# Performance work log

Hardware: AMD Instinct MI355X
Metric: run time of the kernel (lower is better)

The kernel has to match this reference:

```python
import jax, jax.numpy as jnp
import numpy as np

DIM = 1024
HEADS = 16
DIM_HEAD = 64
DIM_INNER = HEADS * DIM_HEAD  # 1024
SEQ = 2048
BATCH = 1


def setup_inputs() -> dict:
    key = jax.random.key(0)
    k1, k2, k3 = jax.random.split(key, 3)
    x = jax.random.normal(k1, (BATCH, SEQ, DIM), dtype=jnp.float32)
    # LinearNoBias(dim, 6*dim_inner): stored as [dim, 6*dim_inner] so fwd is x @ W
    W_qkv = jax.random.normal(k2, (DIM, 6 * DIM_INNER), dtype=jnp.float32) * (DIM ** -0.5)
    W_out = jax.random.normal(k3, (DIM_INNER, DIM), dtype=jnp.float32) * (DIM_INNER ** -0.5)
    return {"x": x, "W_qkv": W_qkv, "W_out": W_out}


def reference(x, W_qkv, W_out):
    b, n, _ = x.shape
    scale = DIM_HEAD ** -0.5

    qkv = x @ W_qkv  # [b, n, 6*h*d]
    qkv = qkv.reshape(b, n, 6, HEADS, DIM_HEAD).transpose(2, 0, 3, 1, 4)  # [6, b, h, n, d]
    qu, ku, vu, qc, kc, vc = qkv

    qc_s = qc * scale
    qu_s = qu * scale

    # strictly-upper-triangular causal mask (True above diagonal)
    causal_mask = jnp.triu(jnp.ones((n, n), dtype=bool), 1)

    # term1: lower-triangular (incl. diag) of qc_s @ vu^T
    term1 = jnp.einsum('bhid,bhjd->bhij', qc_s, vu)
    term1 = jnp.where(causal_mask, 0.0, term1)

    # lookahead: sigmoid of qu_s @ ku^T, strictly upper kept
    lookahead = jax.nn.sigmoid(jnp.einsum('bhid,bhjd->bhij', qu_s, ku))
    lookahead = jnp.where(causal_mask, lookahead, 0.0)

    # Su = term1 @ lookahead^T  (n x n by n x n matmul per head)
    Su = jnp.einsum('bhij,bhkj->bhik', term1, lookahead)

    Sc = jnp.einsum('bhid,bhjd->bhij', qc_s, kc)
    scores = Sc - jax.nn.silu(Su)
    scores = jnp.where(causal_mask, -jnp.inf, scores)

    attn = jax.nn.softmax(scores, axis=-1)
    out = jnp.einsum('bhij,bhjd->bhid', attn, vc)  # [b, h, n, d]

    out = out.transpose(0, 2, 1, 3).reshape(b, n, DIM_INNER)
    return out @ W_out
```

## Files before the change

kernel.cpp:

```cpp
#include <hip/hip_runtime.h>
#include <math.h>

typedef _Float16 f16;
typedef _Float16 f16x4 __attribute__((ext_vector_type(4)));
typedef _Float16 f16x8 __attribute__((ext_vector_type(8)));
typedef float f32x4 __attribute__((ext_vector_type(4)));

#define SEQ   2048
#define DIM   1024
#define NH    16
#define DH    64
#define NCOLS 6144
#define NHSD  (NH*SEQ*DH)
#define NTILE 136
#define MAXS  9
#define SLOTS_PER_HEAD 64

__device__ __forceinline__ int ns2(int a) {
  const int NS2[8] = {1,1,2,3,4,5,7,9};
  return NS2[a];
}
__device__ __forceinline__ int slot_base(int I) {
  const int PF[16] = {0,1,2,3,4,6,8,11,14,18,22,27,32,39,46,55};
  return PF[I];
}

__global__ __launch_bounds__(256) void k_tcast(const float* __restrict__ in, f16* __restrict__ out,
                                               int R, int C) {
  __shared__ f16 t[64 * 66];
  int bc = blockIdx.x, br = blockIdx.y;
  for (int it = 0; it < 16; ++it) {
    int idx = it * 256 + threadIdx.x;
    int r = idx >> 6, c = idx & 63;
    t[r * 66 + c] = (f16)in[(size_t)(br * 64 + r) * C + bc * 64 + c];
  }
  __syncthreads();
  for (int it = 0; it < 16; ++it) {
    int idx = it * 256 + threadIdx.x;
    int oc = idx >> 6, orr = idx & 63;
    out[(size_t)(bc * 64 + oc) * R + br * 64 + orr] = t[orr * 66 + oc];
  }
}

__global__ __launch_bounds__(256) void k_prepA(const float* __restrict__ x, f16* __restrict__ xhT) {
  int kt = blockIdx.x, by = blockIdx.y;
  f16* dst = xhT + ((size_t)(by * 16 + kt) << 13);
  int tid = threadIdx.x;
#pragma unroll
  for (int i = 0; i < 4; ++i) {
    int idx = i * 256 + tid;
    int chunk = idx >> 6, lane = idx & 63;
    int rb = chunk & 7, ks = chunk >> 3;
    int row = by * 128 + rb * 16 + (lane & 15);
    int kk = kt * 64 + ks * 32 + ((lane >> 4) << 3);
    const float* p = x + (size_t)row * DIM + kk;
    float4 lo = *(const float4*)p, hi = *(const float4*)(p + 4);
    f16x8 h;
    h[0] = (f16)lo.x; h[1] = (f16)lo.y; h[2] = (f16)lo.z; h[3] = (f16)lo.w;
    h[4] = (f16)hi.x; h[5] = (f16)hi.y; h[6] = (f16)hi.z; h[7] = (f16)hi.w;
    *(f16x8*)(dst + (size_t)idx * 8) = h;
  }
}

__global__ __launch_bounds__(256) void k_prepB(const float* __restrict__ Wq, f16* __restrict__ WqTf) {
  int kt = blockIdx.x, bx = blockIdx.y;
  f16* dst = WqTf + ((size_t)(bx * 16 + kt) << 13);
  int tid = threadIdx.x;
#pragma unroll
  for (int i = 0; i < 4; ++i) {
    int idx = i * 256 + tid;
    int chunk = idx >> 6, lane = idx & 63;
    int rb = chunk & 7, ks = chunk >> 3;
    int n = bx * 128 + rb * 16 + (lane & 15);
    int kk = kt * 64 + ks * 32 + ((lane >> 4) << 3);
    f16x8 h;
#pragma unroll
    for (int j = 0; j < 8; ++j) h[j] = (f16)Wq[(size_t)(kk + j) * NCOLS + n];
    *(f16x8*)(dst + (size_t)idx * 8) = h;
  }
}

__global__ __launch_bounds__(256) void k_gemm_qkv(const f16* __restrict__ xhT, const f16* __restrict__ WqTf,
                                                  f16* __restrict__ q6, f16* __restrict__ vuF) {
  __shared__ f16 sa[8192];
  __shared__ f16 sb[8192];
  int bx = blockIdx.x, by = blockIdx.y;
  int tid = threadIdx.x, w = tid >> 6, l = tid & 63, q = l >> 4, c = l & 15;
  f32x4 acc[2][8];
  const f32x4 zf = {0.f, 0.f, 0.f, 0.f};
  for (int i = 0; i < 2; ++i) for (int j = 0; j < 8; ++j) acc[i][j] = zf;

  for (int kt = 0; kt < 16; ++kt) {
    const f16* ta = xhT + ((size_t)(by * 16 + kt) << 13);
    const f16* tb = WqTf + ((size_t)(bx * 16 + kt) << 13);
    __syncthreads();
#pragma unroll
    for (int i = 0; i < 4; ++i) {
      int e = (i * 256 + tid) * 8;
      __builtin_amdgcn_global_load_lds((const __attribute__((address_space(1))) void*)(ta + e),
                                       (__attribute__((address_space(3))) void*)(sa + e), 16, 0, 0);
      __builtin_amdgcn_global_load_lds((const __attribute__((address_space(1))) void*)(tb + e),
                                       (__attribute__((address_space(3))) void*)(sb + e), 16, 0, 0);
    }
    __syncthreads();
#pragma unroll
    for (int ks = 0; ks < 2; ++ks) {
      f16x8 af[2], bf[8];
#pragma unroll
      for (int tr = 0; tr < 2; ++tr)
        af[tr] = *(const f16x8*)(sa + ((ks * 8 + w * 2 + tr) * 64 + l) * 8);
#pragma unroll
      for (int tc = 0; tc < 8; ++tc)
        bf[tc] = *(const f16x8*)(sb + ((ks * 8 + tc) * 64 + l) * 8);
#pragma unroll
      for (int tr = 0; tr < 2; ++tr)
#pragma unroll
        for (int tc = 0; tc < 8; ++tc)
          acc[tr][tc] = __builtin_amdgcn_mfma_f32_16x16x32_f16(af[tr], bf[tc], acc[tr][tc], 0, 0, 0);
    }
  }
#pragma unroll
  for (int tr = 0; tr < 2; ++tr)
#pragma unroll
    for (int tc = 0; tc < 8; ++tc)
#pragma unroll
      for (int r = 0; r < 4; ++r) {
        int row = by * 128 + w * 32 + tr * 16 + q * 4 + r;
        int col = bx * 128 + tc * 16 + c;
        float v = acc[tr][tc][r];
        int t = col >> 10, head = (col >> 6) & 15, dh = col & 63;
        if (t == 0 || t == 3) v *= 0.125f;
        f16 hv = (f16)v;
        if (t == 4) {
          size_t addr = (size_t)4 * NHSD + (size_t)head * (SEQ * DH) + ((size_t)(row >> 7) << 13)
                      + (size_t)(((((dh >> 5) << 3) + ((row >> 4) & 7)) * 64
                                  + ((((dh >> 3) & 3) << 4) | (row & 15))) * 8 + (dh & 7));
          q6[addr] = hv;
        } else if (t == 5) {
          size_t addr = (size_t)5 * NHSD + (size_t)head * (SEQ * DH) + ((size_t)(row >> 7) << 13)
                      + (size_t)((((((row >> 5) & 3) << 2) + (dh >> 4)) * 64
                                  + ((((row >> 3) & 3) << 4) | (dh & 15))) * 8 + (row & 7));
          q6[addr] = hv;
        } else if (t == 2) {
          q6[(size_t)2 * NHSD + (size_t)(head * SEQ + row) * DH + dh] = hv;
          size_t fa = ((size_t)(row >> 7) << 13)
                    + (size_t)((((((row >> 5) & 3) << 2) + (dh >> 4)) * 64
                                + ((((row >> 3) & 3) << 4) | (dh & 15))) * 8 + (row & 7));
          vuF[(size_t)head * (SEQ * DH) + fa] = hv;
        } else {
          q6[(size_t)t * NHSD + (size_t)(head * SEQ + row) * DH + dh] = hv;
        }
      }
}

__global__ __launch_bounds__(256) void k_t1lk(const f16* __restrict__ q6, f16* __restrict__ t1dT,
                                              f16* __restrict__ lkT) {
  __shared__ f16 st[128 * 128];
  int head = blockIdx.x / 152;
  int p = blockIdx.x % 152;
  bool is_lk = (p >= 16);
  int RB, CB;
  f16* dst;
  if (is_lk) {
    int p2 = p - 16;
    int K = 0, off = 0;
    while (off + (16 - K) <= p2) { off += 16 - K; ++K; }
    RB = K; CB = K + (p2 - off);
    dst = lkT + ((size_t)(head * NTILE + p2) << 14);
  } else {
    RB = p; CB = p;
    dst = t1dT + ((size_t)(head * 16 + p) << 14);
  }
  const f16* Ah = q6 + (size_t)(is_lk ? 0 : 3) * NHSD + (size_t)head * SEQ * DH;
  const f16* Bh = q6 + (size_t)(is_lk ? 1 : 2) * NHSD + (size_t)head * SEQ * DH;
  int tid = threadIdx.x, w = tid >> 6, l = tid & 63, q = l >> 4, c = l & 15;
  const f32x4 zf = {0.f, 0.f, 0.f, 0.f};
  f32x4 tacc[2][8];
  for (int tr = 0; tr < 2; ++tr) for (int tc = 0; tc < 8; ++tc) tacc[tr][tc] = zf;
#pragma unroll
  for (int ks = 0; ks < 2; ++ks) {
    f16x8 aq[2], bf[8];
#pragma unroll
    for (int tr = 0; tr < 2; ++tr)
      aq[tr] = *(const f16x8*)(Ah + (size_t)(RB * 128 + w * 32 + tr * 16 + c) * DH + ks * 32 + q * 8);
#pragma unroll
    for (int tc = 0; tc < 8; ++tc)
      bf[tc] = *(const f16x8*)(Bh + (size_t)(CB * 128 + tc * 16 + c) * DH + ks * 32 + q * 8);
#pragma unroll
    for (int tr = 0; tr < 2; ++tr)
#pragma unroll
      for (int tc = 0; tc < 8; ++tc)
        tacc[tr][tc] = __builtin_amdgcn_mfma_f32_16x16x32_f16(aq[tr], bf[tc], tacc[tr][tc], 0, 0, 0);
  }
#pragma unroll
  for (int tr = 0; tr < 2; ++tr)
#pragma unroll
    for (int tc = 0; tc < 8; ++tc)
#pragma unroll
      for (int r = 0; r < 4; ++r) {
        int row = w * 32 + tr * 16 + q * 4 + r;
        int col = tc * 16 + c;
        int rg = RB * 128 + row, cg = CB * 128 + col;
        float v = tacc[tr][tc][r];
        f16 ov;
        if (is_lk) ov = (cg > rg) ? (f16)__builtin_amdgcn_rcpf(1.f + __expf(-v)) : (f16)(0.f);
        else       ov = (cg <= rg) ? (f16)v : (f16)(0.f);
        st[(row << 7) + (((col >> 3) ^ (row & 15)) << 3) + (col & 7)] = ov;
      }
  __syncthreads();
#pragma unroll
  for (int i = 0; i < 8; ++i) {
    int ch = i * 256 + tid;
    int ks = ch >> 9, rb = (ch >> 6) & 7, ln = ch & 63;
    int qq = ln >> 4, cc = ln & 15;
    int row = rb * 16 + cc, cchunk = ks * 4 + qq;
    f16x8 v = *(const f16x8*)(st + (row << 7) + ((cchunk ^ (row & 15)) << 3));
    *(f16x8*)(dst + (size_t)ch * 8) = v;
  }
}

__global__ __launch_bounds__(256) void k_prefix(const f16* __restrict__ lkT, const f16* __restrict__ vuF,
                                                f16* __restrict__ PPT) {
  __shared__ f16 lkb[2][16384];
  __shared__ f16 vub[2][8192];
  __shared__ f16 st[8192];
  int head = blockIdx.x >> 4, K = blockIdx.x & 15;
  int offK = 16 * K - (K * (K - 1)) / 2;
  const f16* lkh = lkT + ((size_t)(head * NTILE) << 14);
  const f16* vuh = vuF + (size_t)head * (SEQ * DH);
  f16* pph = PPT + ((size_t)(head * NTILE) << 13);
  int tid = threadIdx.x, w = tid >> 6, l = tid & 63, q = l >> 4, c = l & 15;
  f32x4 acc[2][4];
  const f32x4 zf = {0.f, 0.f, 0.f, 0.f};
  for (int tr = 0; tr < 2; ++tr) for (int tv = 0; tv < 4; ++tv) acc[tr][tv] = zf;
  {
    const f16* lt = lkh + ((size_t)offK << 14);
#pragma unroll
    for (int i = 0; i < 8; ++i) {
      int e = (i * 256 + tid) * 8;
      __builtin_amdgcn_global_load_lds((const __attribute__((address_space(1))) void*)(lt + e),
                                       (__attribute__((address_space(3))) void*)(&lkb[0][0] + e), 16, 0, 0);
    }
    const f16* vt_ = vuh + ((size_t)K << 13);
#pragma unroll
    for (int i = 0; i < 4; ++i) {
      int e = (i * 256 + tid) * 8;
      __builtin_amdgcn_global_load_lds((const __attribute__((address_space(1))) void*)(vt_ + e),
                                       (__attribute__((address_space(3))) void*)(&vub[0][0] + e), 16, 0, 0);
    }
  }
  int pb = 0;
  for (int J = K; J < 16; ++J) {
    __syncthreads();
    if (J < 15) {
      const f16* lt = lkh + ((size_t)(offK + (J + 1 - K)) << 14);
#pragma unroll
      for (int i = 0; i < 8; ++i) {
        int e = (i * 256 + tid) * 8;
        __builtin_amdgcn_global_load_lds((const __attribute__((address_space(1))) void*)(lt + e),
                                         (__attribute__((address_space(3))) void*)(&lkb[pb ^ 1][0] + e), 16, 0, 0);
      }
      const f16* vt_ = vuh + ((size_t)(J + 1) << 13);
#pragma unroll
      for (int i = 0; i < 4; ++i) {
        int e = (i * 256 + tid) * 8;
        __builtin_amdgcn_global_load_lds((const __attribute__((address_space(1))) void*)(vt_ + e),
                                         (__attribute__((address_space(3))) void*)(&vub[pb ^ 1][0] + e), 16, 0, 0);
      }
    }
#pragma unroll
    for (int ks = 0; ks < 4; ++ks) {
      f16x8 af[2], bf[4];
#pragma unroll
      for (int tr = 0; tr < 2; ++tr)
        af[tr] = *(const f16x8*)(&lkb[pb][0] + ((ks * 8 + w * 2 + tr) * 64 + l) * 8);
#pragma unroll
      for (int tv = 0; tv < 4; ++tv)
        bf[tv] = *(const f16x8*)(&vub[pb][0] + ((ks * 4 + tv) * 64 + l) * 8);
#pragma unroll
      for (int tr = 0; tr < 2; ++tr)
#pragma unroll
        for (int tv = 0; tv < 4; ++tv)
          acc[tr][tv] = __builtin_amdgcn_mfma_f32_16x16x32_f16(af[tr], bf[tv], acc[tr][tv], 0, 0, 0);
    }
#pragma unroll
    for (int tr = 0; tr < 2; ++tr)
#pragma unroll
      for (int tv = 0; tv < 4; ++tv)
#pragma unroll
        for (int r = 0; r < 4; ++r) {
          int row = w * 32 + tr * 16 + q * 4 + r;
          int col = tv * 16 + c;
          st[(row << 6) + (((col >> 3) ^ (row & 7)) << 3) + (col & 7)] = (f16)acc[tr][tv][r];
        }
    __syncthreads();
    f16* dst = pph + ((size_t)(offK + (J - K)) << 13);
#pragma unroll
    for (int i = 0; i < 4; ++i) {
      int slot = i * 256 + tid;
      int chunk = slot >> 6, ln = slot & 63;
      int ks2 = chunk >> 3, tc = chunk & 7, qq = ln >> 4, cc = ln & 15;
      int row = tc * 16 + cc, cch = ks2 * 4 + qq;
      f16x8 v = *(const f16x8*)(st + (row << 6) + ((cch ^ (row & 7)) << 3));
      *(f16x8*)(dst + (size_t)slot * 8) = v;
    }
    pb ^= 1;
  }
}

__global__ __launch_bounds__(512, 1) void k_flash(const f16* __restrict__ q6, const f16* __restrict__ t1dT,
                                                  const f16* __restrict__ lkT, const f16* __restrict__ PPT,
                                                  f16* __restrict__ pO, float* __restrict__ pML) {
  __shared__ f16 Sb[2][40960];
  int bid = blockIdx.x;
  int big = bid & 1;
  int rest = bid >> 1;
  int head = ((rest & 7) << 1) | ((rest >> 3) & 1);
  int r2 = 31 - (rest >> 4);
  int a = 0, s = 0;
  {
    int acc = 0;
    for (int aa = 0; aa < 8; ++aa) {
      int si = ns2(aa);
      if (r2 >= acc && r2 < acc + si) { a = aa; s = r2 - acc; }
      acc += si;
    }
  }
  int I1 = 2 * a + 1;
  int S_ = ns2(a);
  int Ktot = I1 + 1;
  int K0 = (Ktot * s) / S_, K1 = (Ktot * (s + 1)) / S_;
  int IB = 2 * a + big;
  int Kbeg = (K0 < IB + 1) ? K0 : IB + 1;
  int Kend = (K1 < IB + 1) ? K1 : IB + 1;

  const f16* qc  = q6 + (size_t)3 * NHSD + (size_t)head * SEQ * DH;
  const f16* kcF = q6 + (size_t)4 * NHSD + (size_t)head * (SEQ * DH);
  const f16* vtF = q6 + (size_t)5 * NHSD + (size_t)head * (SEQ * DH);
  int tid = threadIdx.x, w = tid >> 6, l = tid & 63, q = l >> 4, c = l & 15;
  const f16* lkh = lkT + ((size_t)(head * NTILE) << 14);
  const f16* pph = PPT + ((size_t)(head * NTILE) << 13);
  const f16* t1d = t1dT + ((size_t)(head * 16 + IB) << 14);

  f16x8 a_qc[2];
#pragma unroll
  for (int ks = 0; ks < 2; ++ks)
    a_qc[ks] = *(const f16x8*)(qc + (size_t)(IB * 128 + w * 16 + c) * DH + ks * 32 + q * 8);
  f16x8 a_t1[4];
#pragma unroll
  for (int ks = 0; ks < 4; ++ks)
    a_t1[ks] = *(const f16x8*)(t1d + (size_t)((ks * 8 + w) * 64 + l) * 8);

  f32x4 su[8], oacc[4];
  float m_i[4], l_i[4];
  const f32x4 zf = {0.f, 0.f, 0.f, 0.f};
  for (int tv = 0; tv < 4; ++tv) oacc[tv] = zf;
  for (int r = 0; r < 4; ++r) { m_i[r] = -INFINITY; l_i[r] = 0.f; }

  if (Kbeg < Kend) {
    int K = Kbeg;
    int offK = 16 * K - (K * (K - 1)) / 2;
    f16* D = &Sb[0][0];
    const f16* p1 = lkh + ((size_t)(offK + (IB - K)) << 14);
#pragma unroll
    for (int i = 0; i < 4; ++i) {
      int e = (i * 512 + tid) * 8;
      __builtin_amdgcn_global_load_lds((const __attribute__((address_space(1))) void*)(p1 + e),
                                       (__attribute__((address_space(3))) void*)(D + e), 16, 0, 0);
    }
    if (K < IB) {
      const f16* pp = pph + ((size_t)(offK + (IB - 1 - K)) << 13);
#pragma unroll
      for (int i = 0; i < 2; ++i) {
        int e = (i * 512 + tid) * 8;
        __builtin_amdgcn_global_load_lds((const __attribute__((address_space(1))) void*)(pp + e),
                                         (__attribute__((address_space(3))) void*)(D + 16384 + e), 16, 0, 0);
      }
    }
    const f16* kt_ = kcF + ((size_t)K << 13);
    const f16* vv_ = vtF + ((size_t)K << 13);
#pragma unroll
    for (int i = 0; i < 2; ++i) {
      int e = (i * 512 + tid) * 8;
      __builtin_amdgcn_global_load_lds((const __attribute__((address_space(1))) void*)(kt_ + e),
                                       (__attribute__((address_space(3))) void*)(D + 24576 + e), 16, 0, 0);
      __builtin_amdgcn_global_load_lds((const __attribute__((address_space(1))) void*)(vv_ + e),
                                       (__attribute__((address_space(3))) void*)(D + 32768 + e), 16, 0, 0);
    }
  }

  int cur = 0;
  for (int K = Kbeg; K < Kend; ++K) {
#pragma unroll
    for (int tc = 0; tc < 8; ++tc) su[tc] = zf;

    __syncthreads();

    if (K + 1 < Kend) {
      int Kn = K + 1;
      int offKn = 16 * Kn - (Kn * (Kn - 1)) / 2;
      f16* D = &Sb[cur ^ 1][0];
      const f16* p1 = lkh + ((size_t)(offKn + (IB - Kn)) << 14);
#pragma unroll
      for (int i = 0; i < 4; ++i) {
        int e = (i * 512 + tid) * 8;
        __builtin_amdgcn_global_load_lds((const __attribute__((address_space(1))) void*)(p1 + e),
                                         (__attribute__((address_space(3))) void*)(D + e), 16, 0, 0);
      }
      if (Kn < IB) {
        const f16* pp = pph + ((size_t)(offKn + (IB - 1 - Kn)) << 13);
#pragma unroll
        for (int i = 0; i < 2; ++i) {
          int e = (i * 512 + tid) * 8;
          __builtin_amdgcn_global_load_lds((const __attribute__((address_space(1))) void*)(pp + e),
                                           (__attribute__((address_space(3))) void*)(D + 16384 + e), 16, 0, 0);
        }
      }
      const f16* kt_ = kcF + ((size_t)Kn << 13);
      const f16* vv_ = vtF + ((size_t)Kn << 13);
#pragma unroll
      for (int i = 0; i < 2; ++i) {
        int e = (i * 512 + tid) * 8;
        __builtin_amdgcn_global_load_lds((const __attribute__((address_space(1))) void*)(kt_ + e),
                                         (__attribute__((address_space(3))) void*)(D + 24576 + e), 16, 0, 0);
        __builtin_amdgcn_global_load_lds((const __attribute__((address_space(1))) void*)(vv_ + e),
                                         (__attribute__((address_space(3))) void*)(D + 32768 + e), 16, 0, 0);
      }
    }

    f16* bufc = &Sb[cur][0];
    if (K < IB) {
      const f16* ppb = bufc + 16384;
#pragma unroll
      for (int ks = 0; ks < 2; ++ks) {
        f16x8 bf[8];
#pragma unroll
        for (int tc = 0; tc < 8; ++tc)
          bf[tc] = *(const f16x8*)(ppb + ((ks * 8 + tc) * 64 + l) * 8);
#pragma unroll
        for (int tc = 0; tc < 8; ++tc)
          su[tc] = __builtin_amdgcn_mfma_f32_16x16x32_f16(a_qc[ks], bf[tc], su[tc], 0, 0, 0);
      }
    }
    {
      __builtin_amdgcn_s_setprio(1);
#pragma unroll
      for (int ks = 0; ks < 4; ++ks) {
        f16x8 bf[8];
#pragma unroll
        for (int tc = 0; tc < 8; ++tc)
          bf[tc] = *(const f16x8*)(bufc + ((ks * 8 + tc) * 64 + l) * 8);
#pragma unroll
        for (int tc = 0; tc < 8; ++tc)
          su[tc] = __builtin_amdgcn_mfma_f32_16x16x32_f16(a_t1[ks], bf[tc], su[tc], 0, 0, 0);
      }
      __builtin_amdgcn_s_setprio(0);
    }
#pragma unroll
    for (int tc = 0; tc < 8; ++tc)
#pragma unroll
      for (int r = 0; r < 4; ++r) {
        float v = su[tc][r];
        su[tc][r] = -v * __builtin_amdgcn_rcpf(1.f + __expf(-v));
      }
    {
      const f16* skc = bufc + 24576;
#pragma unroll
      for (int ks = 0; ks < 2; ++ks) {
        f16x8 bk[8];
#pragma unroll
        for (int tc = 0; tc < 8; ++tc)
          bk[tc] = *(const f16x8*)(skc + ((ks * 8 + tc) * 64 + l) * 8);
#pragma unroll
        for (int tc = 0; tc < 8; ++tc)
          su[tc] = __builtin_amdgcn_mfma_f32_16x16x32_f16(a_qc[ks], bk[tc], su[tc], 0, 0, 0);
      }
    }
    if (K == IB) {
#pragma unroll
      for (int tc = 0; tc < 8; ++tc)
#pragma unroll
        for (int r = 0; r < 4; ++r) {
          int rg = w * 16 + q * 4 + r;
          int cg = tc * 16 + c;
          if (cg > rg) su[tc][r] = -INFINITY;
        }
    }
#pragma unroll
    for (int r = 0; r < 4; ++r) {
      float mx = su[0][r];
#pragma unroll
      for (int tc = 1; tc < 8; ++tc) mx = fmaxf(mx, su[tc][r]);
      mx = fmaxf(mx, __shfl_xor(mx, 1)); mx = fmaxf(mx, __shfl_xor(mx, 2));
      mx = fmaxf(mx, __shfl_xor(mx, 4)); mx = fmaxf(mx, __shfl_xor(mx, 8));
      float mnew  = fmaxf(m_i[r], mx);
      float alpha = __expf(m_i[r] - mnew);
      float ssum = 0.f;
#pragma unroll
      for (int tc = 0; tc < 8; ++tc) {
        float pp = __expf(su[tc][r] - mnew);
        su[tc][r] = pp;
        ssum += pp;
      }
      ssum += __shfl_xor(ssum, 1); ssum += __shfl_xor(ssum, 2);
      ssum += __shfl_xor(ssum, 4); ssum += __shfl_xor(ssum, 8);
      l_i[r] = l_i[r] * alpha + ssum;
      m_i[r] = mnew;
#pragma unroll
      for (int tv = 0; tv < 4; ++tv) oacc[tv][r] *= alpha;
    }
    asm volatile("s_waitcnt lgkmcnt(0)" ::: "memory");
    __builtin_amdgcn_sched_barrier(0);
    __builtin_amdgcn_s_barrier();
    __builtin_amdgcn_sched_barrier(0);
#pragma unroll
    for (int tc = 0; tc < 8; ++tc)
#pragma unroll
      for (int r = 0; r < 4; ++r) {
        int row = w * 16 + q * 4 + r;
        int col = tc * 16 + c;
        bufc[(row << 7) + (((col >> 3) ^ (row & 15)) << 3) + (col & 7)] = (f16)su[tc][r];
      }
    {
      const f16* svt = bufc + 32768;
#pragma unroll
      for (int ks = 0; ks < 4; ++ks) {
        int ck = ks * 4 + q;
        f16x8 ap, bv[4];
        ap = *(const f16x8*)(bufc + ((w * 16 + c) << 7) + ((ck ^ c) << 3));
#pragma unroll
        for (int tv = 0; tv < 4; ++tv)
          bv[tv] = *(const f16x8*)(svt + ((ks * 4 + tv) * 64 + l) * 8);
#pragma unroll
        for (int tv = 0; tv < 4; ++tv)
          oacc[tv] = __builtin_amdgcn_mfma_f32_16x16x32_f16(ap, bv[tv], oacc[tv], 0, 0, 0);
      }
    }
    cur ^= 1;
  }

  int slot = head * SLOTS_PER_HEAD + slot_base(IB) + s;
  f16* po = pO + (size_t)slot * (128 * 64);
  float* pml = pML + (size_t)slot * 256;
  if (c == 0) {
#pragma unroll
    for (int r = 0; r < 4; ++r) {
      int row = w * 16 + q * 4 + r;
      pml[row] = m_i[r];
      pml[128 + row] = l_i[r];
    }
  }
#pragma unroll
  for (int tv = 0; tv < 4; ++tv)
#pragma unroll
    for (int r = 0; r < 4; ++r) {
      int row = w * 16 + q * 4 + r;
      int col = tv * 16 + c;
      po[row * 64 + col] = (f16)oacc[tv][r];
    }
}

__global__ __launch_bounds__(256) void k_merge(const f16* __restrict__ pO, const float* __restrict__ pML,
                                               f16* __restrict__ oh) {
  int head = blockIdx.x >> 4, I = blockIdx.x & 15;
  int S_ = ns2(I >> 1);
  int tid = threadIdx.x;
  int row = tid >> 1, half = tid & 1;
  int base = head * SLOTS_PER_HEAD + slot_base(I);
  float m[MAXS], lv[MAXS];
  float mstar = -INFINITY;
#pragma unroll
  for (int s = 0; s < MAXS; ++s)
    if (s < S_) {
      m[s] = pML[(size_t)(base + s) * 256 + row];
      lv[s] = pML[(size_t)(base + s) * 256 + 128 + row];
      mstar = fmaxf(mstar, m[s]);
    }
  float wt[MAXS];
  float lsum = 0.f;
#pragma unroll
  for (int s = 0; s < MAXS; ++s)
    if (s < S_) {
      wt[s] = __expf(m[s] - mstar);
      lsum += lv[s] * wt[s];
    }
  float rinv = __builtin_amdgcn_rcpf(lsum);
#pragma unroll
  for (int cc = 0; cc < 32; cc += 8) {
    float acc[8] = {0.f, 0.f, 0.f, 0.f, 0.f, 0.f, 0.f, 0.f};
#pragma unroll
    for (int s = 0; s < MAXS; ++s)
      if (s < S_) {
        f16x8 v = *(const f16x8*)(pO + (size_t)(base + s) * 8192 + row * 64 + half * 32 + cc);
#pragma unroll
        for (int e = 0; e < 8; ++e) acc[e] += wt[s] * (float)v[e];
      }
    f16x8 o;
#pragma unroll
    for (int e = 0; e < 8; ++e) o[e] = (f16)(acc[e] * rinv);
    *(f16x8*)(oh + (size_t)(I * 128 + row) * DIM + head * 64 + half * 32 + cc) = o;
  }
}

__global__ __launch_bounds__(256) void k_gemm_out(const f16* __restrict__ A, const f16* __restrict__ B,
                                                  float* __restrict__ out) {
  __shared__ f16 sa[128 * 72];
  __shared__ f16 sb[128 * 72];
  int bx = blockIdx.x, by = blockIdx.y;
  int tid = threadIdx.x, w = tid >> 6, l = tid & 63, q = l >> 4, c = l & 15;
  f32x4 acc[2][8];
  const f32x4 zf = {0.f, 0.f, 0.f, 0.f};
  for (int i = 0; i < 2; ++i) for (int j = 0; j < 8; ++j) acc[i][j] = zf;
  for (int kt = 0; kt < DIM / 64; ++kt) {
    __syncthreads();
#pragma unroll
    for (int it = 0; it < 4; ++it) {
      int idx = it * 256 + tid; int r = idx >> 3, ch = idx & 7;
      *(float4*)(sa + r * 72 + ch * 8) = *(const float4*)(A + (size_t)(by * 128 + r) * DIM + kt * 64 + ch * 8);
      *(float4*)(sb + r * 72 + ch * 8) = *(const float4*)(B + (size_t)(bx * 128 + r) * DIM + kt * 64 + ch * 8);
    }
    __syncthreads();
#pragma unroll
    for (int ks = 0; ks < 2; ++ks) {
      f16x8 af[2], bf[8];
#pragma unroll
      for (int tr = 0; tr < 2; ++tr) af[tr] = *(const f16x8*)(sa + (w * 32 + tr * 16 + c) * 72 + ks * 32 + q * 8);
#pragma unroll
      for (int tc = 0; tc < 8; ++tc) bf[tc] = *(const f16x8*)(sb + (tc * 16 + c) * 72 + ks * 32 + q * 8);
#pragma unroll
      for (int tr = 0; tr < 2; ++tr)
#pragma unroll
        for (int tc = 0; tc < 8; ++tc)
          acc[tr][tc] = __builtin_amdgcn_mfma_f32_16x16x32_f16(af[tr], bf[tc], acc[tr][tc], 0, 0, 0);
    }
  }
#pragma unroll
  for (int tr = 0; tr < 2; ++tr)
#pragma unroll
    for (int tc = 0; tc < 8; ++tc)
#pragma unroll
      for (int r = 0; r < 4; ++r) {
        int row = by * 128 + w * 32 + tr * 16 + q * 4 + r;
        int col = bx * 128 + tc * 16 + c;
        out[(size_t)row * DIM + col] = acc[tr][tc][r];
      }
}

extern "C" void kernel_launch(void* const* d_in, const int* in_sizes, int n_in,
                              void* d_out, int out_size, void* d_ws, size_t ws_size,
                              hipStream_t stream) {
  const float* x  = (const float*)d_in[0];
  const float* Wq = (const float*)d_in[1];
  const float* Wo = (const float*)d_in[2];
  float* out = (float*)d_out;

  f16* ws = (f16*)d_ws;
  size_t off = 0;
  f16* q6   = ws + off; off += (size_t)6 * NHSD;
  f16* vuF  = ws + off; off += (size_t)NHSD;
  f16* xhT  = ws + off; off += (size_t)SEQ * DIM;
  f16* WqTf = ws + off; off += (size_t)NCOLS * DIM;
  f16* WoT  = ws + off; off += (size_t)DIM * DIM;
  f16* oh   = ws + off; off += (size_t)SEQ * DIM;
  f16* pO   = ws + off; off += (size_t)NH * SLOTS_PER_HEAD * 128 * 64;
  f16* lkT  = ws + off; off += (size_t)NH * NTILE * 128 * 128;
  f16* t1dT = ws + off; off += (size_t)NH * 16 * 128 * 128;
  f16* PPT  = ws + off; off += (size_t)NH * NTILE * 128 * 64;
  float* pML = (float*)(ws + off); off += (size_t)NH * SLOTS_PER_HEAD * 256 * 2;

  k_prepA<<<dim3(16, 16), 256, 0, stream>>>(x, xhT);
  k_prepB<<<dim3(16, 48), 256, 0, stream>>>(Wq, WqTf);
  k_tcast<<<dim3(DIM / 64, DIM / 64), 256, 0, stream>>>(Wo, WoT, DIM, DIM);
  k_gemm_qkv<<<dim3(NCOLS / 128, SEQ / 128), 256, 0, stream>>>(xhT, WqTf, q6, vuF);
  k_t1lk<<<NH * 152, 256, 0, stream>>>(q6, t1dT, lkT);
  k_prefix<<<NH * 16, 256, 0, stream>>>(lkT, vuF, PPT);
  k_flash<<<NH * 64, 512, 0, stream>>>(q6, t1dT, lkT, PPT, pO, pML);
  k_merge<<<NH * 16, 256, 0, stream>>>(pO, pML, oh);
  k_gemm_out<<<dim3(DIM / 128, SEQ / 128), 256, 0, stream>>>(oh, WoT, out);
}
```

Baseline: 315.2 us.

## Fuse weight/input prep kernels and coalesce Wq transpose; narrow output GEMM tiles

Merges the three preprocessing kernels (x cast, W_qkv transpose-cast, W_out transpose-cast) into one launch dispatched by block index, which removes two kernel launches. The W_qkv transpose now reads rows with coalesced float4 loads and transposes through shared memory, replacing the previous strided per-element global reads. The output GEMM tile shrinks from 128x128 to 128x64, doubling the grid from 128 to 256 blocks so more CUs are busy, at the cost of re-reading the A tile more often.

```diff
diff --git a/kernel.cpp b/kernel.cpp
--- a/kernel.cpp
+++ b/kernel.cpp
@@ -25,58 +25,68 @@
   return PF[I];
 }
 
-__global__ __launch_bounds__(256) void k_tcast(const float* __restrict__ in, f16* __restrict__ out,
-                                               int R, int C) {
-  __shared__ f16 t[64 * 66];
-  int bc = blockIdx.x, br = blockIdx.y;
-  for (int it = 0; it < 16; ++it) {
-    int idx = it * 256 + threadIdx.x;
-    int r = idx >> 6, c = idx & 63;
-    t[r * 66 + c] = (f16)in[(size_t)(br * 64 + r) * C + bc * 64 + c];
-  }
-  __syncthreads();
-  for (int it = 0; it < 16; ++it) {
-    int idx = it * 256 + threadIdx.x;
-    int oc = idx >> 6, orr = idx & 63;
-    out[(size_t)(bc * 64 + oc) * R + br * 64 + orr] = t[orr * 66 + oc];
-  }
-}
-
-__global__ __launch_bounds__(256) void k_prepA(const float* __restrict__ x, f16* __restrict__ xhT) {
-  int kt = blockIdx.x, by = blockIdx.y;
-  f16* dst = xhT + ((size_t)(by * 16 + kt) << 13);
+__global__ __launch_bounds__(256) void k_prep(const float* __restrict__ x,  f16* __restrict__ xhT,
+                                              const float* __restrict__ Wq, f16* __restrict__ WqTf,
+                                              const float* __restrict__ Wo, f16* __restrict__ WoT) {
+  __shared__ f16 sw[64 * 130];
+  int b = blockIdx.x;
   int tid = threadIdx.x;
-#pragma unroll
-  for (int i = 0; i < 4; ++i) {
-    int idx = i * 256 + tid;
-    int chunk = idx >> 6, lane = idx & 63;
-    int rb = chunk & 7, ks = chunk >> 3;
-    int row = by * 128 + rb * 16 + (lane & 15);
-    int kk = kt * 64 + ks * 32 + ((lane >> 4) << 3);
-    const float* p = x + (size_t)row * DIM + kk;
-    float4 lo = *(const float4*)p, hi = *(const float4*)(p + 4);
-    f16x8 h;
-    h[0] = (f16)lo.x; h[1] = (f16)lo.y; h[2] = (f16)lo.z; h[3] = (f16)lo.w;
-    h[4] = (f16)hi.x; h[5] = (f16)hi.y; h[6] = (f16)hi.z; h[7] = (f16)hi.w;
-    *(f16x8*)(dst + (size_t)idx * 8) = h;
-  }
-}
-
-__global__ __launch_bounds__(256) void k_prepB(const float* __restrict__ Wq, f16* __restrict__ WqTf) {
-  int kt = blockIdx.x, bx = blockIdx.y;
-  f16* dst = WqTf + ((size_t)(bx * 16 + kt) << 13);
-  int tid = threadIdx.x;
-#pragma unroll
-  for (int i = 0; i < 4; ++i) {
-    int idx = i * 256 + tid;
-    int chunk = idx >> 6, lane = idx & 63;
-    int rb = chunk & 7, ks = chunk >> 3;
-    int n = bx * 128 + rb * 16 + (lane & 15);
-    int kk = kt * 64 + ks * 32 + ((lane >> 4) << 3);
-    f16x8 h;
-#pragma unroll
-    for (int j = 0; j < 8; ++j) h[j] = (f16)Wq[(size_t)(kk + j) * NCOLS + n];
-    *(f16x8*)(dst + (size_t)idx * 8) = h;
+  if (b < 256) {
+    int kt = b & 15, by = b >> 4;
+    f16* dst = xhT + ((size_t)(by * 16 + kt) << 13);
+#pragma unroll
+    for (int i = 0; i < 4; ++i) {
+      int idx = i * 256 + tid;
+      int chunk = idx >> 6, lane = idx & 63;
+      int rb = chunk & 7, ks = chunk >> 3;
+      int row = by * 128 + rb * 16 + (lane & 15);
+      int kk = kt * 64 + ks * 32 + ((lane >> 4) << 3);
+      const float* p = x + (size_t)row * DIM + kk;
+      float4 lo = *(const float4*)p, hi = *(const float4*)(p + 4);
+      f16x8 h;
+      h[0] = (f16)lo.x; h[1] = (f16)lo.y; h[2] = (f16)lo.z; h[3] = (f16)lo.w;
+      h[4] = (f16)hi.x; h[5] = (f16)hi.y; h[6] = (f16)hi.z; h[7] = (f16)hi.w;
+      *(f16x8*)(dst + (size_t)idx * 8) = h;
+    }
+  } else if (b < 1024) {
+    int t = b - 256;
+    int kt = t & 15, bx = t >> 4;
+#pragma unroll
+    for (int it = 0; it < 8; ++it) {
+      int idx = it * 256 + tid;
+      int r = idx >> 5, c4 = idx & 31;
+      float4 v = *(const float4*)(Wq + (size_t)(kt * 64 + r) * NCOLS + bx * 128 + c4 * 4);
+      f16* d = sw + r * 130 + c4 * 4;
+      d[0] = (f16)v.x; d[1] = (f16)v.y; d[2] = (f16)v.z; d[3] = (f16)v.w;
+    }
+    __syncthreads();
+    f16* dst = WqTf + ((size_t)(bx * 16 + kt) << 13);
+#pragma unroll
+    for (int i = 0; i < 4; ++i) {
+      int idx = i * 256 + tid;
+      int chunk = idx >> 6, lane = idx & 63;
+      int rb = chunk & 7, ks = chunk >> 3;
+      int nl = rb * 16 + (lane & 15);
+      int kl = ks * 32 + ((lane >> 4) << 3);
+      f16x8 h;
+#pragma unroll
+      for (int j = 0; j < 8; ++j) h[j] = sw[(kl + j) * 130 + nl];
+      *(f16x8*)(dst + (size_t)idx * 8) = h;
+    }
+  } else {
+    int t = b - 1024;
+    int bc = t & 15, br = t >> 4;
+    for (int it = 0; it < 16; ++it) {
+      int idx = it * 256 + tid;
+      int r = idx >> 6, c = idx & 63;
+      sw[r * 66 + c] = (f16)Wo[(size_t)(br * 64 + r) * DIM + bc * 64 + c];
+    }
+    __syncthreads();
+    for (int it = 0; it < 16; ++it) {
+      int idx = it * 256 + tid;
+      int oc = idx >> 6, orr = idx & 63;
+      WoT[(size_t)(bc * 64 + oc) * DIM + br * 64 + orr] = sw[orr * 66 + oc];
+    }
   }
 }
 
@@ -605,43 +615,47 @@
 __global__ __launch_bounds__(256) void k_gemm_out(const f16* __restrict__ A, const f16* __restrict__ B,
                                                   float* __restrict__ out) {
   __shared__ f16 sa[128 * 72];
-  __shared__ f16 sb[128 * 72];
+  __shared__ f16 sb[64 * 72];
   int bx = blockIdx.x, by = blockIdx.y;
   int tid = threadIdx.x, w = tid >> 6, l = tid & 63, q = l >> 4, c = l & 15;
-  f32x4 acc[2][8];
+  f32x4 acc[2][4];
   const f32x4 zf = {0.f, 0.f, 0.f, 0.f};
-  for (int i = 0; i < 2; ++i) for (int j = 0; j < 8; ++j) acc[i][j] = zf;
+  for (int i = 0; i < 2; ++i) for (int j = 0; j < 4; ++j) acc[i][j] = zf;
   for (int kt = 0; kt < DIM / 64; ++kt) {
     __syncthreads();
 #pragma unroll
     for (int it = 0; it < 4; ++it) {
       int idx = it * 256 + tid; int r = idx >> 3, ch = idx & 7;
       *(float4*)(sa + r * 72 + ch * 8) = *(const float4*)(A + (size_t)(by * 128 + r) * DIM + kt * 64 + ch * 8);
-      *(float4*)(sb + r * 72 + ch * 8) = *(const float4*)(B + (size_t)(bx * 128 + r) * DIM + kt * 64 + ch * 8);
+    }
+#pragma unroll
+    for (int it = 0; it < 2; ++it) {
+      int idx = it * 256 + tid; int r = idx >> 3, ch = idx & 7;
+      *(float4*)(sb + r * 72 + ch * 8) = *(const float4*)(B + (size_t)(bx * 64 + r) * DIM + kt * 64 + ch * 8);
     }
     __syncthreads();
 #pragma unroll
     for (int ks = 0; ks < 2; ++ks) {
-      f16x8 af[2], bf[8];
+      f16x8 af[2], bf[4];
 #pragma unroll
       for (int tr = 0; tr < 2; ++tr) af[tr] = *(const f16x8*)(sa + (w * 32 + tr * 16 + c) * 72 + ks * 32 + q * 8);
 #pragma unroll
-      for (int tc = 0; tc < 8; ++tc) bf[tc] = *(const f16x8*)(sb + (tc * 16 + c) * 72 + ks * 32 + q * 8);
+      for (int tc = 0; tc < 4; ++tc) bf[tc] = *(const f16x8*)(sb + (tc * 16 + c) * 72 + ks * 32 + q * 8);
 #pragma unroll
       for (int tr = 0; tr < 2; ++tr)
 #pragma unroll
-        for (int tc = 0; tc < 8; ++tc)
+        for (int tc = 0; tc < 4; ++tc)
           acc[tr][tc] = __builtin_amdgcn_mfma_f32_16x16x32_f16(af[tr], bf[tc], acc[tr][tc], 0, 0, 0);
     }
   }
 #pragma unroll
   for (int tr = 0; tr < 2; ++tr)
 #pragma unroll
-    for (int tc = 0; tc < 8; ++tc)
+    for (int tc = 0; tc < 4; ++tc)
 #pragma unroll
       for (int r = 0; r < 4; ++r) {
         int row = by * 128 + w * 32 + tr * 16 + q * 4 + r;
-        int col = bx * 128 + tc * 16 + c;
+        int col = bx * 64 + tc * 16 + c;
         out[(size_t)row * DIM + col] = acc[tr][tc][r];
       }
 }
@@ -668,13 +682,11 @@
   f16* PPT  = ws + off; off += (size_t)NH * NTILE * 128 * 64;
   float* pML = (float*)(ws + off); off += (size_t)NH * SLOTS_PER_HEAD * 256 * 2;
 
-  k_prepA<<<dim3(16, 16), 256, 0, stream>>>(x, xhT);
-  k_prepB<<<dim3(16, 48), 256, 0, stream>>>(Wq, WqTf);
-  k_tcast<<<dim3(DIM / 64, DIM / 64), 256, 0, stream>>>(Wo, WoT, DIM, DIM);
+  k_prep<<<1280, 256, 0, stream>>>(x, xhT, Wq, WqTf, Wo, WoT);
   k_gemm_qkv<<<dim3(NCOLS / 128, SEQ / 128), 256, 0, stream>>>(xhT, WqTf, q6, vuF);
   k_t1lk<<<NH * 152, 256, 0, stream>>>(q6, t1dT, lkT);
   k_prefix<<<NH * 16, 256, 0, stream>>>(lkT, vuF, PPT);
   k_flash<<<NH * 64, 512, 0, stream>>>(q6, t1dT, lkT, PPT, pO, pML);
   k_merge<<<NH * 16, 256, 0, stream>>>(pO, pML, oh);
-  k_gemm_out<<<dim3(DIM / 128, SEQ / 128), 256, 0, stream>>>(oh, WoT, out);
-}
+  k_gemm_out<<<dim3(DIM / 64, SEQ / 128), 256, 0, stream>>>(oh, WoT, out);
+}
```

After: 337.4 us. 1.07x slower.

## Double-buffer QKV GEMM LDS tiles and stage weight transpose through shared memory

Applied to the files above, without the earlier changes.

The QKV projection GEMM now keeps two LDS buffers for the A and B tiles. The next k-tile is loaded with global_load_lds while MFMAs run on the current one, so global memory latency overlaps with compute. The weight-prep kernel first reads the W_qkv tile into padded shared memory with coalesced float4 loads, then gathers the transposed f16 fragments from LDS, replacing strided global reads. The cost is double the LDS per GEMM block, which may lower occupancy.

```diff
diff --git a/kernel.cpp b/kernel.cpp
--- a/kernel.cpp
+++ b/kernel.cpp
@@ -63,61 +63,86 @@
 }
 
 __global__ __launch_bounds__(256) void k_prepB(const float* __restrict__ Wq, f16* __restrict__ WqTf) {
+  __shared__ f16 sw[64 * 130];
   int kt = blockIdx.x, bx = blockIdx.y;
+  int tid = threadIdx.x;
+#pragma unroll
+  for (int it = 0; it < 8; ++it) {
+    int idx = it * 256 + tid;
+    int r = idx >> 5, c4 = idx & 31;
+    float4 v = *(const float4*)(Wq + (size_t)(kt * 64 + r) * NCOLS + bx * 128 + c4 * 4);
+    f16* d = sw + r * 130 + c4 * 4;
+    d[0] = (f16)v.x; d[1] = (f16)v.y; d[2] = (f16)v.z; d[3] = (f16)v.w;
+  }
+  __syncthreads();
   f16* dst = WqTf + ((size_t)(bx * 16 + kt) << 13);
-  int tid = threadIdx.x;
 #pragma unroll
   for (int i = 0; i < 4; ++i) {
     int idx = i * 256 + tid;
     int chunk = idx >> 6, lane = idx & 63;
     int rb = chunk & 7, ks = chunk >> 3;
-    int n = bx * 128 + rb * 16 + (lane & 15);
-    int kk = kt * 64 + ks * 32 + ((lane >> 4) << 3);
+    int nl = rb * 16 + (lane & 15);
+    int kl = ks * 32 + ((lane >> 4) << 3);
     f16x8 h;
 #pragma unroll
-    for (int j = 0; j < 8; ++j) h[j] = (f16)Wq[(size_t)(kk + j) * NCOLS + n];
+    for (int j = 0; j < 8; ++j) h[j] = sw[(kl + j) * 130 + nl];
     *(f16x8*)(dst + (size_t)idx * 8) = h;
   }
 }
 
 __global__ __launch_bounds__(256) void k_gemm_qkv(const f16* __restrict__ xhT, const f16* __restrict__ WqTf,
                                                   f16* __restrict__ q6, f16* __restrict__ vuF) {
-  __shared__ f16 sa[8192];
-  __shared__ f16 sb[8192];
+  __shared__ f16 sa[2][8192];
+  __shared__ f16 sb[2][8192];
   int bx = blockIdx.x, by = blockIdx.y;
   int tid = threadIdx.x, w = tid >> 6, l = tid & 63, q = l >> 4, c = l & 15;
   f32x4 acc[2][8];
   const f32x4 zf = {0.f, 0.f, 0.f, 0.f};
   for (int i = 0; i < 2; ++i) for (int j = 0; j < 8; ++j) acc[i][j] = zf;
 
-  for (int kt = 0; kt < 16; ++kt) {
-    const f16* ta = xhT + ((size_t)(by * 16 + kt) << 13);
-    const f16* tb = WqTf + ((size_t)(bx * 16 + kt) << 13);
-    __syncthreads();
+  {
+    const f16* ta = xhT + ((size_t)(by * 16) << 13);
+    const f16* tb = WqTf + ((size_t)(bx * 16) << 13);
 #pragma unroll
     for (int i = 0; i < 4; ++i) {
       int e = (i * 256 + tid) * 8;
       __builtin_amdgcn_global_load_lds((const __attribute__((address_space(1))) void*)(ta + e),
-                                       (__attribute__((address_space(3))) void*)(sa + e), 16, 0, 0);
+                                       (__attribute__((address_space(3))) void*)(&sa[0][0] + e), 16, 0, 0);
       __builtin_amdgcn_global_load_lds((const __attribute__((address_space(1))) void*)(tb + e),
-                                       (__attribute__((address_space(3))) void*)(sb + e), 16, 0, 0);
-    }
+                                       (__attribute__((address_space(3))) void*)(&sb[0][0] + e), 16, 0, 0);
+    }
+  }
+  int cur = 0;
+  for (int kt = 0; kt < 16; ++kt) {
     __syncthreads();
+    if (kt + 1 < 16) {
+      const f16* ta = xhT + ((size_t)(by * 16 + kt + 1) << 13);
+      const f16* tb = WqTf + ((size_t)(bx * 16 + kt + 1) << 13);
+#pragma unroll
+      for (int i = 0; i < 4; ++i) {
+        int e = (i * 256 + tid) * 8;
+        __builtin_amdgcn_global_load_lds((const __attribute__((address_space(1))) void*)(ta + e),
+                                         (__attribute__((address_space(3))) void*)(&sa[cur ^ 1][0] + e), 16, 0, 0);
+        __builtin_amdgcn_global_load_lds((const __attribute__((address_space(1))) void*)(tb + e),
+                                         (__attribute__((address_space(3))) void*)(&sb[cur ^ 1][0] + e), 16, 0, 0);
+      }
+    }
 #pragma unroll
     for (int ks = 0; ks < 2; ++ks) {
       f16x8 af[2], bf[8];
 #pragma unroll
       for (int tr = 0; tr < 2; ++tr)
-        af[tr] = *(const f16x8*)(sa + ((ks * 8 + w * 2 + tr) * 64 + l) * 8);
+        af[tr] = *(const f16x8*)(&sa[cur][0] + ((ks * 8 + w * 2 + tr) * 64 + l) * 8);
 #pragma unroll
       for (int tc = 0; tc < 8; ++tc)
-        bf[tc] = *(const f16x8*)(sb + ((ks * 8 + tc) * 64 + l) * 8);
+        bf[tc] = *(const f16x8*)(&sb[cur][0] + ((ks * 8 + tc) * 64 + l) * 8);
 #pragma unroll
       for (int tr = 0; tr < 2; ++tr)
 #pragma unroll
         for (int tc = 0; tc < 8; ++tc)
           acc[tr][tc] = __builtin_amdgcn_mfma_f32_16x16x32_f16(af[tr], bf[tc], acc[tr][tc], 0, 0, 0);
     }
+    cur ^= 1;
   }
 #pragma unroll
   for (int tr = 0; tr < 2; ++tr)
```

Result: slower. 323.2 us (+2.5%).
